# Optimization experiments

Hardware: AMD Instinct MI355X
Metric: run time of the kernel (lower is better)

The kernel has to match this reference:

```python
import jax, jax.numpy as jnp
import numpy as np

B, S, D, H = 2, 2048, 2048, 16
DH = D // H  # 128 head dim
ROPE_THETA = 10000.0
LN_EPS = 1e-5


def setup_inputs() -> dict:
    key = jax.random.key(0)
    k1, k2, k3 = jax.random.split(key, 3)
    positions = jnp.broadcast_to(jnp.arange(S, dtype=jnp.int64), (B, S))
    hidden_states = jax.random.normal(k1, (B, S, D), dtype=jnp.float32)
    w_qkv = jax.random.normal(k2, (D, 3 * D), dtype=jnp.float32) * 0.02
    w_out = jax.random.normal(k3, (D, D), dtype=jnp.float32) * 0.02
    return {"positions": positions, "hidden_states": hidden_states,
            "w_qkv": w_qkv, "w_out": w_out}


def _rope(x, positions):
    # NeoX-style rotary (vLLM get_rope default): rotate split halves.
    # x: [B, S, H, DH], positions: [B, S]
    half = DH // 2
    inv_freq = 1.0 / (ROPE_THETA ** (jnp.arange(0, half, dtype=jnp.float32) / half))
    ang = positions.astype(jnp.float32)[..., None] * inv_freq  # [B, S, half]
    cos = jnp.cos(ang)[:, :, None, :]  # [B, S, 1, half]
    sin = jnp.sin(ang)[:, :, None, :]
    x1, x2 = x[..., :half], x[..., half:]
    return jnp.concatenate([x1 * cos - x2 * sin, x2 * cos + x1 * sin], axis=-1)


def reference(positions, hidden_states, w_qkv, w_out):
    # LayerNorm with no affine params (elementwise_affine=False)
    mu = jnp.mean(hidden_states, axis=-1, keepdims=True)
    var = jnp.mean(jnp.square(hidden_states - mu), axis=-1, keepdims=True)
    x = (hidden_states - mu) * jax.lax.rsqrt(var + LN_EPS)

    qkv = jnp.einsum('bsd,de->bse', x, w_qkv)  # [B, S, 3D]
    q, k, v = jnp.split(qkv, 3, axis=-1)
    q = q.reshape(B, S, H, DH)
    k = k.reshape(B, S, H, DH)
    v = v.reshape(B, S, H, DH)

    q = _rope(q, positions)
    k = _rope(k, positions)

    scale = DH ** -0.5
    scores = jnp.einsum('bqhd,bkhd->bhqk', q, k) * scale  # [B, H, S, S]
    causal = jnp.tril(jnp.ones((S, S), dtype=bool))
    scores = jnp.where(causal, scores, jnp.finfo(scores.dtype).min)
    probs = jax.nn.softmax(scores, axis=-1)
    attn = jnp.einsum('bhqk,bkhd->bqhd', probs, v).reshape(B, S, D)

    return jnp.einsum('bsd,de->bse', attn, w_out)
```

## Files before the change

### kernel.cpp

```cpp
#include <hip/hip_runtime.h>


typedef __bf16 bf16x8 __attribute__((ext_vector_type(8)));
typedef float f32x4 __attribute__((ext_vector_type(4)));

__device__ __forceinline__ unsigned short f2bf(float f) {
  unsigned u = __builtin_bit_cast(unsigned, f);
  u = u + 0x7fffu + ((u >> 16) & 1u);
  return (unsigned short)(u >> 16);
}
__device__ __forceinline__ float bf2f(unsigned short h) {
  unsigned u = ((unsigned)h) << 16;
  return __builtin_bit_cast(float, u);
}

#define GLD_LDS16(gp, lp)                                                      \
  __builtin_amdgcn_global_load_lds((__attribute__((address_space(1))) void*)(gp), \
                                   (__attribute__((address_space(3))) void*)(lp), \
                                   16, 0, 0)

__global__ __launch_bounds__(256) void prep_kernel(const float* __restrict__ hs,
                                                   const float* __restrict__ wqkv,
                                                   const float* __restrict__ wout,
                                                   unsigned short* __restrict__ xb,
                                                   unsigned short* __restrict__ wqkvT,
                                                   unsigned short* __restrict__ woutT) {
  const int tid = threadIdx.x;
  int bx = blockIdx.x;
  if (bx < 4096) {
    const float* rp = hs + (size_t)bx * 2048;
    const float4 v0 = ((const float4*)rp)[tid];
    const float4 v1 = ((const float4*)rp)[tid + 256];
    float s  = v0.x + v0.y + v0.z + v0.w + v1.x + v1.y + v1.z + v1.w;
    float ss = v0.x*v0.x + v0.y*v0.y + v0.z*v0.z + v0.w*v0.w
             + v1.x*v1.x + v1.y*v1.y + v1.z*v1.z + v1.w*v1.w;
#pragma unroll
    for (int m = 1; m < 64; m <<= 1) { s += __shfl_xor(s, m); ss += __shfl_xor(ss, m); }
    __shared__ float rs[4], rss[4];
    if ((tid & 63) == 0) { rs[tid >> 6] = s; rss[tid >> 6] = ss; }
    __syncthreads();
    s  = rs[0] + rs[1] + rs[2] + rs[3];
    ss = rss[0] + rss[1] + rss[2] + rss[3];
    const float mean = s * (1.0f / 2048.0f);
    const float var  = ss * (1.0f / 2048.0f) - mean * mean;
    const float inv  = rsqrtf(var + 1e-5f);
    ushort4 o0, o1;
    o0.x = f2bf((v0.x - mean) * inv); o0.y = f2bf((v0.y - mean) * inv);
    o0.z = f2bf((v0.z - mean) * inv); o0.w = f2bf((v0.w - mean) * inv);
    o1.x = f2bf((v1.x - mean) * inv); o1.y = f2bf((v1.y - mean) * inv);
    o1.z = f2bf((v1.z - mean) * inv); o1.w = f2bf((v1.w - mean) * inv);
    ushort4* op = (ushort4*)(xb + (size_t)bx * 2048);
    op[tid] = o0; op[tid + 256] = o1;
    return;
  }
  bx -= 4096;
  const int bxx = bx & 255, byy = bx >> 8;
  const float* in;
  unsigned short* out;
  int N, n0;
  if (bxx < 192) { in = wqkv; out = wqkvT; N = 6144; n0 = bxx * 32; }
  else           { in = wout; out = woutT; N = 2048; n0 = (bxx - 192) * 32; }
  const int k0 = byy * 32;
  const int tx = tid & 31, ty = tid >> 5;
  __shared__ float t[32][33];
#pragma unroll
  for (int i = 0; i < 4; i++)
    t[ty + i * 8][tx] = in[(size_t)(k0 + ty + i * 8) * N + n0 + tx];
  __syncthreads();
#pragma unroll
  for (int i = 0; i < 4; i++)
    out[(size_t)(n0 + ty + i * 8) * 2048 + k0 + tx] = f2bf(t[tx][ty + i * 8]);
}

template <int OUT_BF16>
__global__ __launch_bounds__(256) void gemm_bt(const unsigned short* __restrict__ A,
                                               const unsigned short* __restrict__ Bt,
                                               void* __restrict__ Cv,
                                               int M, int N, int K) {
  __shared__ alignas(16) unsigned short sA[128 * 64];
  __shared__ alignas(16) unsigned short sB[128 * 64];
  const int tid = threadIdx.x;
  const int lane = tid & 63, wave = tid >> 6;
  const int wm = wave >> 1, wn = wave & 1;
  const int ln15 = lane & 15, quad = lane >> 4;
  const size_t m0 = (size_t)blockIdx.y * 128, n0 = (size_t)blockIdx.x * 128;
  const unsigned short* Ag = A + m0 * (size_t)K;
  const unsigned short* Bg = Bt + n0 * (size_t)K;
  const int lr8 = lane >> 3;
  const int sc8 = ((lane & 7) ^ (lr8 & 7)) * 8;
  const int xk = ln15 & 7;

  f32x4 acc[4][4];
#pragma unroll
  for (int mi = 0; mi < 4; mi++)
#pragma unroll
    for (int ni = 0; ni < 4; ni++) acc[mi][ni] = (f32x4){0.f, 0.f, 0.f, 0.f};

  const int iters = K >> 6;
  for (int kt = 0; kt < iters; ++kt) {
    const int kb = kt * 64;
    __syncthreads();
#pragma unroll
    for (int i = 0; i < 4; i++) {
      const int c = wave * 4 + i;
      const int row = c * 8 + lr8;
      GLD_LDS16(Ag + (size_t)row * K + kb + sc8, &sA[c * 512]);
      GLD_LDS16(Bg + (size_t)row * K + kb + sc8, &sB[c * 512]);
    }
    __syncthreads();
#pragma unroll
    for (int ks = 0; ks < 2; ks++) {
      bf16x8 af[4], bf[4];
#pragma unroll
      for (int mi = 0; mi < 4; mi++)
        af[mi] = *(const bf16x8*)&sA[(wm * 64 + mi * 16 + ln15) * 64 +
                                     ((ks * 4 + quad) ^ xk) * 8];
#pragma unroll
      for (int ni = 0; ni < 4; ni++)
        bf[ni] = *(const bf16x8*)&sB[(wn * 64 + ni * 16 + ln15) * 64 +
                                     ((ks * 4 + quad) ^ xk) * 8];
#pragma unroll
      for (int mi = 0; mi < 4; mi++)
#pragma unroll
        for (int ni = 0; ni < 4; ni++)
          acc[mi][ni] = __builtin_amdgcn_mfma_f32_16x16x32_bf16(af[mi], bf[ni], acc[mi][ni], 0, 0, 0);
    }
  }
#pragma unroll
  for (int mi = 0; mi < 4; mi++)
#pragma unroll
    for (int ni = 0; ni < 4; ni++) {
      const size_t col = n0 + wn * 64 + ni * 16 + ln15;
#pragma unroll
      for (int r = 0; r < 4; r++) {
        const size_t row = m0 + wm * 64 + mi * 16 + quad * 4 + r;
        if (OUT_BF16)
          ((unsigned short*)Cv)[row * N + col] = f2bf(acc[mi][ni][r]);
        else
          ((float*)Cv)[row * N + col] = acc[mi][ni][r];
      }
    }
}

__global__ __launch_bounds__(256) void rv_kernel(const unsigned short* __restrict__ qkv,
                                                 unsigned short* __restrict__ Qo,
                                                 unsigned short* __restrict__ Ko,
                                                 unsigned short* __restrict__ VT) {
  const int tid = threadIdx.x;
  const int bx = blockIdx.x;
  if (bx < 2048) {
    const int t = bx * 256 + tid;
    const int g = t & 7;
    const int h = (t >> 3) & 15;
    const int row = t >> 7;
    const int s = row & 2047;
    const size_t base = (size_t)row * 6144 + h * 128 + g * 8;
    const bf16x8 q1 = *(const bf16x8*)&qkv[base];
    const bf16x8 q2 = *(const bf16x8*)&qkv[base + 64];
    const bf16x8 k1 = *(const bf16x8*)&qkv[base + 2048];
    const bf16x8 k2 = *(const bf16x8*)&qkv[base + 2048 + 64];
    const float qscale = 0.08838834764831845f;
    bf16x8 oq1, oq2, ok1, ok2;
#pragma unroll
    for (int j = 0; j < 8; j++) {
      const int i = g * 8 + j;
      const float freq = exp2f(-(float)i * (13.287712379549449f / 64.0f));
      float rev = (float)s * freq * 0.15915494309189535f;
      rev -= floorf(rev);
      const float ar = rev * 6.283185307179586f;
      const float sn = __sinf(ar), cs = __cosf(ar);
      const float a1 = (float)q1[j], a2 = (float)q2[j];
      const float b1 = (float)k1[j], b2 = (float)k2[j];
      oq1[j] = (__bf16)((a1 * cs - a2 * sn) * qscale);
      oq2[j] = (__bf16)((a2 * cs + a1 * sn) * qscale);
      ok1[j] = (__bf16)(b1 * cs - b2 * sn);
      ok2[j] = (__bf16)(b2 * cs + b1 * sn);
    }
    const size_t ob = ((size_t)(((row >> 11) << 4) + h) * 2048 + s) * 128 + g * 8;
    *(bf16x8*)&Qo[ob]      = oq1;
    *(bf16x8*)&Qo[ob + 64] = oq2;
    *(bf16x8*)&Ko[ob]      = ok1;
    *(bf16x8*)&Ko[ob + 64] = ok2;
    return;
  }
  const int idx = bx - 2048;
  const int s0 = (idx & 63) * 32;
  const int d0 = ((idx >> 6) & 3) * 32;
  const int bh = idx >> 8, b = bh >> 4, h = bh & 15;
  const int tx = tid & 31, ty = tid >> 5;
  __shared__ unsigned short t[32][34];
#pragma unroll
  for (int i = 0; i < 4; i++)
    t[ty + i * 8][tx] =
        qkv[(size_t)(b * 2048 + s0 + ty + i * 8) * 6144 + 4096 + h * 128 + d0 + tx];
  __syncthreads();
#pragma unroll
  for (int i = 0; i < 4; i++)
    VT[((size_t)bh * 128 + d0 + ty + i * 8) * 2048 + s0 + tx] = t[tx][ty + i * 8];
}

__global__ __launch_bounds__(256) void flash_kernel(const unsigned short* __restrict__ Q,
                                                    const unsigned short* __restrict__ Kbuf,
                                                    const unsigned short* __restrict__ VT,
                                                    unsigned short* __restrict__ attn) {
  __shared__ alignas(16) unsigned short sK[2][64 * 128];
  __shared__ alignas(16) unsigned short sVT[2][128 * 64];
  __shared__ alignas(16) unsigned short sP[64 * 72];

  const int bh = blockIdx.y;
  const int b = bh >> 4, h = bh & 15;
  const int tid = threadIdx.x;
  const int lane = tid & 63, w = tid >> 6;
  const int ln15 = lane & 15, quad = lane >> 4;

  const unsigned short* Qg = Q + (size_t)bh * 2048 * 128;
  const unsigned short* Kg = Kbuf + (size_t)bh * 2048 * 128;
  const unsigned short* Vg = VT + (size_t)bh * 128 * 2048;

  const float L2E = 1.44269504088896f;
  bf16x8 onesf;
#pragma unroll
  for (int j = 0; j < 8; j++) onesf[j] = (__bf16)1.0f;

  const int kcrow = (lane >> 4);
  const int kch = (lane & 15);
  const int vcrow = (lane >> 3);
  const int vch = (lane & 7);

#pragma unroll 1
  for (int t = 0; t < 2; t++) {
    const int qt = t ? (31 - (int)blockIdx.x) : (int)blockIdx.x;
    const int q0 = qt * 64;

    bf16x8 qf[4];
#pragma unroll
    for (int ks = 0; ks < 4; ks++)
      qf[ks] = *(const bf16x8*)&Qg[(size_t)(q0 + w * 16 + ln15) * 128 + ks * 32 + quad * 8];

    f32x4 o[8], ol;
#pragma unroll
    for (int nd = 0; nd < 8; nd++) o[nd] = (f32x4){0.f, 0.f, 0.f, 0.f};
    ol = (f32x4){0.f, 0.f, 0.f, 0.f};
    float mrow[4];
#pragma unroll
    for (int r = 0; r < 4; r++) mrow[r] = -1e30f;

    __syncthreads();
#pragma unroll
    for (int i = 0; i < 4; i++) {
      const int c = w * 4 + i;
      const int row = c * 4 + kcrow;
      GLD_LDS16(Kg + (size_t)row * 128 + (kch ^ (row & 15)) * 8, &sK[0][c * 512]);
    }
#pragma unroll
    for (int i = 0; i < 4; i++) {
      const int c = w * 4 + i;
      const int row = c * 8 + vcrow;
      GLD_LDS16(Vg + (size_t)row * 2048 + (vch ^ (row & 7)) * 8, &sVT[0][c * 512]);
    }

#pragma unroll 1
    for (int j = 0; j <= qt; j++) {
      const int cur = j & 1;
      __syncthreads();
      if (j < qt) {
        const int k0n = (j + 1) * 64;
        const int nxt = cur ^ 1;
#pragma unroll
        for (int i = 0; i < 4; i++) {
          const int c = w * 4 + i;
          const int row = c * 4 + kcrow;
          GLD_LDS16(Kg + (size_t)(k0n + row) * 128 + (kch ^ (row & 15)) * 8, &sK[nxt][c * 512]);
        }
#pragma unroll
        for (int i = 0; i < 4; i++) {
          const int c = w * 4 + i;
          const int row = c * 8 + vcrow;
          GLD_LDS16(Vg + (size_t)row * 2048 + k0n + (vch ^ (row & 7)) * 8, &sVT[nxt][c * 512]);
        }
      }

      f32x4 sc[4];
#pragma unroll
      for (int ni = 0; ni < 4; ni++) sc[ni] = (f32x4){0.f, 0.f, 0.f, 0.f};
#pragma unroll
      for (int ks = 0; ks < 4; ks++) {
        bf16x8 bk[4];
#pragma unroll
        for (int ni = 0; ni < 4; ni++) {
          const int row = ni * 16 + ln15;
          const int ch = (ks * 4 + quad) ^ (row & 15);
          bk[ni] = *(const bf16x8*)&sK[cur][row * 128 + ch * 8];
        }
#pragma unroll
        for (int ni = 0; ni < 4; ni++)
          sc[ni] = __builtin_amdgcn_mfma_f32_16x16x32_bf16(qf[ks], bk[ni], sc[ni], 0, 0, 0);
      }

      float mt[4] = {-1e30f, -1e30f, -1e30f, -1e30f};
      if (j == qt) {
        const int k0 = j * 64;
#pragma unroll
        for (int ni = 0; ni < 4; ni++) {
          const int key = k0 + ni * 16 + ln15;
#pragma unroll
          for (int r = 0; r < 4; r++) {
            const int qrow = q0 + w * 16 + quad * 4 + r;
            float v = sc[ni][r];
            if (key > qrow) v = -1e30f;
            sc[ni][r] = v;
            mt[r] = fmaxf(mt[r], v);
          }
        }
      } else {
#pragma unroll
        for (int ni = 0; ni < 4; ni++)
#pragma unroll
          for (int r = 0; r < 4; r++) mt[r] = fmaxf(mt[r], sc[ni][r]);
      }
#pragma unroll
      for (int r = 0; r < 4; r++) {
        float m = mt[r];
        m = fmaxf(m, __shfl_xor(m, 1));
        m = fmaxf(m, __shfl_xor(m, 2));
        m = fmaxf(m, __shfl_xor(m, 4));
        m = fmaxf(m, __shfl_xor(m, 8));
        const float mnew = fmaxf(mrow[r], m);
        const float alpha = exp2f((mrow[r] - mnew) * L2E);
        mrow[r] = mnew;
#pragma unroll
        for (int ni = 0; ni < 4; ni++)
          sc[ni][r] = exp2f((sc[ni][r] - mnew) * L2E);
        ol[r] *= alpha;
#pragma unroll
        for (int nd = 0; nd < 8; nd++) o[nd][r] *= alpha;
      }
#pragma unroll
      for (int ni = 0; ni < 4; ni++)
#pragma unroll
        for (int r = 0; r < 4; r++)
          sP[(w * 16 + quad * 4 + r) * 72 + ni * 16 + ln15] = f2bf(sc[ni][r]);

      bf16x8 pf[2];
#pragma unroll
      for (int kk = 0; kk < 2; kk++)
        pf[kk] = *(const bf16x8*)&sP[(w * 16 + ln15) * 72 + kk * 32 + quad * 8];
#pragma unroll
      for (int kk = 0; kk < 2; kk++) {
#pragma unroll
        for (int nd = 0; nd < 8; nd++) {
          const int row = nd * 16 + ln15;
          const int ch = (kk * 4 + quad) ^ (row & 7);
          const bf16x8 bv = *(const bf16x8*)&sVT[cur][row * 64 + ch * 8];
          o[nd] = __builtin_amdgcn_mfma_f32_16x16x32_bf16(pf[kk], bv, o[nd], 0, 0, 0);
        }
        ol = __builtin_amdgcn_mfma_f32_16x16x32_bf16(pf[kk], onesf, ol, 0, 0, 0);
      }
    }

#pragma unroll
    for (int r = 0; r < 4; r++) {
      const float inv = 1.0f / ol[r];
      const int qrow = q0 + w * 16 + quad * 4 + r;
#pragma unroll
      for (int nd = 0; nd < 8; nd++) {
        const int d = nd * 16 + ln15;
        attn[((size_t)(b * 2048 + qrow)) * 2048 + h * 128 + d] = f2bf(o[nd][r] * inv);
      }
    }
  }
}

extern "C" void kernel_launch(void* const* d_in, const int* in_sizes, int n_in,
                              void* d_out, int out_size, void* d_ws, size_t ws_size,
                              hipStream_t stream) {
  const float* hs   = (const float*)d_in[1];
  const float* wqkv = (const float*)d_in[2];
  const float* wout = (const float*)d_in[3];
  float* out = (float*)d_out;
  char* ws = (char*)d_ws;

  unsigned short* x_bf  = (unsigned short*)(ws);
  unsigned short* wqkvT = (unsigned short*)(ws + 16777216);
  unsigned short* woutT = (unsigned short*)(ws + 41943040);
  unsigned short* qkv   = (unsigned short*)(ws + 50331648);
  unsigned short* Qb    = (unsigned short*)(ws + 100663296);
  unsigned short* Kb    = (unsigned short*)(ws + 117440512);
  unsigned short* VT    = wqkvT;
  unsigned short* attn  = x_bf;

  prep_kernel<<<4096 + 16384, 256, 0, stream>>>(hs, wqkv, wout, x_bf, wqkvT, woutT);
  gemm_bt<1><<<dim3(48, 32), 256, 0, stream>>>(x_bf, wqkvT, (void*)qkv, 4096, 6144, 2048);
  rv_kernel<<<2048 + 8192, 256, 0, stream>>>(qkv, Qb, Kb, VT);
  flash_kernel<<<dim3(16, 32), 256, 0, stream>>>(Qb, Kb, VT, attn);
  gemm_bt<0><<<dim3(16, 32), 256, 0, stream>>>(attn, woutT, (void*)out, 4096, 2048, 2048);
}
```

Measured before the change: 416.2 us.

## Vectorize transpose tiles, defer softmax rescale, and raise MFMA wave priority

The weight-transpose and V-transpose paths move to 64x64 tiles with float4/8-wide loads and 16-byte stores, cutting block count and narrow scalar memory traffic. The flash kernel skips the running-max rescale of the output accumulators unless some row's max grows by more than a threshold, removing many exp/multiply ops per tile. MFMA sections are wrapped in s_setprio to favour matrix issue. Deferred rescale lets exponents run up to 2^8 above the stored max, which slightly changes numerics but stays within fp32 range.

```diff
diff --git a/kernel.cpp b/kernel.cpp
--- a/kernel.cpp
+++ b/kernel.cpp
@@ -3,15 +3,12 @@
 
 typedef __bf16 bf16x8 __attribute__((ext_vector_type(8)));
 typedef float f32x4 __attribute__((ext_vector_type(4)));
+typedef unsigned short u16x8 __attribute__((ext_vector_type(8)));
 
 __device__ __forceinline__ unsigned short f2bf(float f) {
   unsigned u = __builtin_bit_cast(unsigned, f);
   u = u + 0x7fffu + ((u >> 16) & 1u);
   return (unsigned short)(u >> 16);
-}
-__device__ __forceinline__ float bf2f(unsigned short h) {
-  unsigned u = ((unsigned)h) << 16;
-  return __builtin_bit_cast(float, u);
 }
 
 #define GLD_LDS16(gp, lp)                                                      \
@@ -54,22 +51,33 @@
     return;
   }
   bx -= 4096;
-  const int bxx = bx & 255, byy = bx >> 8;
   const float* in;
   unsigned short* out;
-  int N, n0;
-  if (bxx < 192) { in = wqkv; out = wqkvT; N = 6144; n0 = bxx * 32; }
-  else           { in = wout; out = woutT; N = 2048; n0 = (bxx - 192) * 32; }
-  const int k0 = byy * 32;
-  const int tx = tid & 31, ty = tid >> 5;
-  __shared__ float t[32][33];
-#pragma unroll
-  for (int i = 0; i < 4; i++)
-    t[ty + i * 8][tx] = in[(size_t)(k0 + ty + i * 8) * N + n0 + tx];
+  int N, nt, kt;
+  if (bx < 3072) { in = wqkv; out = wqkvT; N = 6144; nt = bx % 96; kt = bx / 96; }
+  else { bx -= 3072; in = wout; out = woutT; N = 2048; nt = bx & 31; kt = bx >> 5; }
+  const int n0 = nt * 64, k0 = kt * 64;
+  __shared__ float t[64 * 65];
+  const int tx4 = (tid & 15) * 4, ty = tid >> 4;
+#pragma unroll
+  for (int i = 0; i < 4; i++) {
+    const int k = ty + i * 16;
+    const float4 v = *(const float4*)&in[(size_t)(k0 + k) * N + n0 + tx4];
+    t[(tx4 + 0) * 65 + k] = v.x;
+    t[(tx4 + 1) * 65 + k] = v.y;
+    t[(tx4 + 2) * 65 + k] = v.z;
+    t[(tx4 + 3) * 65 + k] = v.w;
+  }
   __syncthreads();
-#pragma unroll
-  for (int i = 0; i < 4; i++)
-    out[(size_t)(n0 + ty + i * 8) * 2048 + k0 + tx] = f2bf(t[tx][ty + i * 8]);
+  const int kc = (tid & 7) * 8, nr = tid >> 3;
+#pragma unroll
+  for (int i = 0; i < 2; i++) {
+    const int n = nr + i * 32;
+    u16x8 o;
+#pragma unroll
+    for (int j = 0; j < 8; j++) o[j] = f2bf(t[n * 65 + kc + j]);
+    *(u16x8*)&out[(size_t)(n0 + n) * 2048 + k0 + kc] = o;
+  }
 }
 
 template <int OUT_BF16>
@@ -184,19 +192,29 @@
     return;
   }
   const int idx = bx - 2048;
-  const int s0 = (idx & 63) * 32;
-  const int d0 = ((idx >> 6) & 3) * 32;
-  const int bh = idx >> 8, b = bh >> 4, h = bh & 15;
-  const int tx = tid & 31, ty = tid >> 5;
-  __shared__ unsigned short t[32][34];
-#pragma unroll
-  for (int i = 0; i < 4; i++)
-    t[ty + i * 8][tx] =
-        qkv[(size_t)(b * 2048 + s0 + ty + i * 8) * 6144 + 4096 + h * 128 + d0 + tx];
+  const int s0 = (idx & 31) * 64;
+  const int d0 = ((idx >> 5) & 1) * 64;
+  const int bh = idx >> 6, b = bh >> 4, h = bh & 15;
+  __shared__ unsigned short t[64 * 65];
+  const int tx8 = (tid & 7) * 8, ty = tid >> 3;
+#pragma unroll
+  for (int i = 0; i < 2; i++) {
+    const int s = ty + i * 32;
+    const u16x8 v = *(const u16x8*)&qkv[(size_t)(b * 2048 + s0 + s) * 6144 +
+                                        4096 + h * 128 + d0 + tx8];
+#pragma unroll
+    for (int j = 0; j < 8; j++) t[(tx8 + j) * 65 + s] = v[j];
+  }
   __syncthreads();
-#pragma unroll
-  for (int i = 0; i < 4; i++)
-    VT[((size_t)bh * 128 + d0 + ty + i * 8) * 2048 + s0 + tx] = t[tx][ty + i * 8];
+  const int sc8 = (tid & 7) * 8, dr = tid >> 3;
+#pragma unroll
+  for (int i = 0; i < 2; i++) {
+    const int d = dr + i * 32;
+    u16x8 o;
+#pragma unroll
+    for (int j = 0; j < 8; j++) o[j] = t[d * 65 + sc8 + j];
+    *(u16x8*)&VT[((size_t)bh * 128 + d0 + d) * 2048 + s0 + sc8] = o;
+  }
 }
 
 __global__ __launch_bounds__(256) void flash_kernel(const unsigned short* __restrict__ Q,
@@ -283,6 +301,7 @@
       f32x4 sc[4];
 #pragma unroll
       for (int ni = 0; ni < 4; ni++) sc[ni] = (f32x4){0.f, 0.f, 0.f, 0.f};
+      __builtin_amdgcn_s_setprio(1);
 #pragma unroll
       for (int ks = 0; ks < 4; ks++) {
         bf16x8 bk[4];
@@ -296,6 +315,7 @@
         for (int ni = 0; ni < 4; ni++)
           sc[ni] = __builtin_amdgcn_mfma_f32_16x16x32_bf16(qf[ks], bk[ni], sc[ni], 0, 0, 0);
       }
+      __builtin_amdgcn_s_setprio(0);
 
       float mt[4] = {-1e30f, -1e30f, -1e30f, -1e30f};
       if (j == qt) {
@@ -318,6 +338,7 @@
 #pragma unroll
           for (int r = 0; r < 4; r++) mt[r] = fmaxf(mt[r], sc[ni][r]);
       }
+      float m4[4];
 #pragma unroll
       for (int r = 0; r < 4; r++) {
         float m = mt[r];
@@ -325,16 +346,27 @@
         m = fmaxf(m, __shfl_xor(m, 2));
         m = fmaxf(m, __shfl_xor(m, 4));
         m = fmaxf(m, __shfl_xor(m, 8));
-        const float mnew = fmaxf(mrow[r], m);
-        const float alpha = exp2f((mrow[r] - mnew) * L2E);
-        mrow[r] = mnew;
+        m4[r] = m;
+      }
+      const bool defer = (m4[0] <= mrow[0] + 8.0f) & (m4[1] <= mrow[1] + 8.0f) &
+                         (m4[2] <= mrow[2] + 8.0f) & (m4[3] <= mrow[3] + 8.0f);
+      if (!__all(defer)) {
+#pragma unroll
+        for (int r = 0; r < 4; r++) {
+          const float mnew = fmaxf(mrow[r], m4[r]);
+          const float alpha = exp2f((mrow[r] - mnew) * L2E);
+          mrow[r] = mnew;
+          ol[r] *= alpha;
+#pragma unroll
+          for (int nd = 0; nd < 8; nd++) o[nd][r] *= alpha;
+        }
+      }
+#pragma unroll
+      for (int r = 0; r < 4; r++)
 #pragma unroll
         for (int ni = 0; ni < 4; ni++)
-          sc[ni][r] = exp2f((sc[ni][r] - mnew) * L2E);
-        ol[r] *= alpha;
-#pragma unroll
-        for (int nd = 0; nd < 8; nd++) o[nd][r] *= alpha;
-      }
+          sc[ni][r] = exp2f((sc[ni][r] - mrow[r]) * L2E);
+
 #pragma unroll
       for (int ni = 0; ni < 4; ni++)
 #pragma unroll
@@ -345,6 +377,7 @@
 #pragma unroll
       for (int kk = 0; kk < 2; kk++)
         pf[kk] = *(const bf16x8*)&sP[(w * 16 + ln15) * 72 + kk * 32 + quad * 8];
+      __builtin_amdgcn_s_setprio(1);
 #pragma unroll
       for (int kk = 0; kk < 2; kk++) {
 #pragma unroll
@@ -356,6 +389,7 @@
         }
         ol = __builtin_amdgcn_mfma_f32_16x16x32_bf16(pf[kk], onesf, ol, 0, 0, 0);
       }
+      __builtin_amdgcn_s_setprio(0);
     }
 
 #pragma unroll
@@ -389,9 +423,9 @@
   unsigned short* VT    = wqkvT;
   unsigned short* attn  = x_bf;
 
-  prep_kernel<<<4096 + 16384, 256, 0, stream>>>(hs, wqkv, wout, x_bf, wqkvT, woutT);
+  prep_kernel<<<4096 + 4096, 256, 0, stream>>>(hs, wqkv, wout, x_bf, wqkvT, woutT);
   gemm_bt<1><<<dim3(48, 32), 256, 0, stream>>>(x_bf, wqkvT, (void*)qkv, 4096, 6144, 2048);
-  rv_kernel<<<2048 + 8192, 256, 0, stream>>>(qkv, Qb, Kb, VT);
+  rv_kernel<<<2048 + 2048, 256, 0, stream>>>(qkv, Qb, Kb, VT);
   flash_kernel<<<dim3(16, 32), 256, 0, stream>>>(Qb, Kb, VT, attn);
   gemm_bt<0><<<dim3(16, 32), 256, 0, stream>>>(attn, woutT, (void*)out, 4096, 2048, 2048);
 }
```

After: 399.7 us. 4.0% less time.
